# Kernel tuning notes

Measured on AMD Instinct MI355X. Metric: run time of the kernel, lower is better.

## Reference

```python
import jax, jax.numpy as jnp
import numpy as np


def setup_inputs() -> dict:
    key = jax.random.key(0)
    ks = jax.random.split(key, 7)
    S, A, I, H = 2000, 1000, 5, 32
    return {
        "g": jax.random.normal(ks[0], (S, A, I), dtype=jnp.float32),
        "W1": jax.random.normal(ks[1], (A, I, H), dtype=jnp.float32) * (1.0 / np.sqrt(I)),
        "b1": jax.random.normal(ks[2], (A, H), dtype=jnp.float32) * 0.01,
        "W2": jax.random.normal(ks[3], (A, H, H), dtype=jnp.float32) * (1.0 / np.sqrt(H)),
        "b2": jax.random.normal(ks[4], (A, H), dtype=jnp.float32) * 0.01,
        "W3": jax.random.normal(ks[5], (A, H, 1), dtype=jnp.float32) * (1.0 / np.sqrt(H)),
        "b3": jax.random.normal(ks[6], (A, 1), dtype=jnp.float32) * 0.01,
    }


def reference(g, W1, b1, W2, b2, W3, b3):
    # Batched equivalent of the nested per-struct / per-atom Python loop:
    # each atom `a` has its own tiny MLP (5 -> 32 -> 32 -> 1, tanh),
    # applied to g[s, a] for every structure s. Grouped-GEMM form:
    # s = struct, a = atom, i/h/o = feature dims.
    h1 = jnp.tanh(jnp.einsum('sai,aih->sah', g, W1) + b1[None, :, :])
    h2 = jnp.tanh(jnp.einsum('sah,aho->sao', h1, W2) + b2[None, :, :])
    e = jnp.einsum('sah,aho->sao', h2, W3) + b3[None, :, :]
    # e_nn has shape [n_struct, n_atoms], matching the torch buffer.
    return e[..., 0]
```

## Files before the change

### kernel.cpp

```cpp
#include <hip/hip_runtime.h>
#include <hip/hip_bf16.h>

#define NS_TOT 2000
#define NA 1000
#define NI 5
#define NH 32
#define SHALF 1000

typedef __attribute__((ext_vector_type(2)))  float f32x2;
typedef __attribute__((ext_vector_type(8)))  short short8;
typedef __attribute__((ext_vector_type(16))) float f32x16;

struct f4pair  { f32x2 a, b; };
struct accpair { f32x2 p[8]; };

__device__ __forceinline__ f32x2 tanh_pk(f32x2 X) {
    f32x2 z = X * X;
    f32x2 n = (z + 105.0f) * z + 945.0f;
    f32x2 d = (z * 15.0f + 420.0f) * z + 945.0f;
    f32x2 r;
    r.x = __builtin_amdgcn_rcpf(d.x);
    r.y = __builtin_amdgcn_rcpf(d.y);
    f32x2 t = X * n * r;
    t.x = __builtin_amdgcn_fmed3f(t.x, -1.0f, 1.0f);
    t.y = __builtin_amdgcn_fmed3f(t.y, -1.0f, 1.0f);
    return t;
}

__device__ __forceinline__ unsigned short f2bf_rne(float x) {
    unsigned u = __float_as_uint(x);
    unsigned r = u + 0x7FFFu + ((u >> 16) & 1u);
    return (unsigned short)(r >> 16);
}
__device__ __forceinline__ unsigned pack2(float a, float b) {
    __hip_bfloat162 p = __float22bfloat162_rn(make_float2(a, b));
    unsigned u; __builtin_memcpy(&u, &p, 4); return u;
}
__device__ __forceinline__ unsigned tanh2_pack(float a, float b) {
    f32x2 X = {a, b};
    f32x2 t = tanh_pk(X);
    return pack2(t.x, t.y);
}

__global__ __attribute__((amdgpu_flat_work_group_size(256, 256),
                          amdgpu_waves_per_eu(4, 8)))
void mlp_mfma(
    const float* __restrict__ g,
    const float* __restrict__ W1, const float* __restrict__ b1,
    const float* __restrict__ W2, const float* __restrict__ b2,
    const float* __restrict__ W3, const float* __restrict__ b3,
    float* __restrict__ out)
{
    const int bid   = blockIdx.x;
    const int araw  = bid % NA;
    const int chunk = bid / NA;
    const int a = (araw >> 3) + 125 * (araw & 7);
    const int t = threadIdx.x;
    const int lane = t & 63, wid = t >> 6;
    const int l31 = lane & 31, half = lane >> 5;

    const int sbase_blk = chunk * SHALF;
    const int send      = sbase_blk + SHALF;

    __shared__ __align__(16) unsigned short sW2T[NH * NH];
    __shared__ __align__(16) unsigned short sW1T[NH * 8];
    __shared__ __align__(16) float sB2[NH];
    __shared__ __align__(16) float sW3[NH];

    for (int idx = t; idx < NH * NH; idx += 256) {
        const int i = idx >> 5, j = idx & 31;
        sW2T[j * NH + i] = f2bf_rne(W2[(size_t)a * NH * NH + idx]);
    }
    if (t < NH) {
        sB2[t] = b2[a * NH + t];
        sW3[t] = W3[a * NH + t];
        const int m = t;
        #pragma unroll
        for (int i = 0; i < NI; ++i)
            sW1T[m * 8 + i] = f2bf_rne(W1[(size_t)a * NI * NH + i * NH + m]);
        sW1T[m * 8 + 5] = f2bf_rne(b1[a * NH + m]);
        sW1T[m * 8 + 6] = 0;
        sW1T[m * 8 + 7] = 0;
    }
    __syncthreads();

    const short8 zero8 = {0,0,0,0,0,0,0,0};
    const short8 w1ld = __builtin_bit_cast(short8, *(const uint4*)(sW1T + l31 * 8));
    const short8 afl1 = half ? zero8 : w1ld;
    const short8 af0 = __builtin_bit_cast(short8, *(const uint4*)(sW2T + l31 * NH + half * 8));
    const short8 af1 = __builtin_bit_cast(short8, *(const uint4*)(sW2T + l31 * NH + 16 + half * 8));
    const float4 b2q0 = ((const float4*)sB2)[0 + half];
    const float4 b2q1 = ((const float4*)sB2)[2 + half];
    const float4 b2q2 = ((const float4*)sB2)[4 + half];
    const float4 b2q3 = ((const float4*)sB2)[6 + half];
    const float4 w3q0 = ((const float4*)sW3)[0 + half];
    const float4 w3q1 = ((const float4*)sW3)[2 + half];
    const float4 w3q2 = ((const float4*)sW3)[4 + half];
    const float4 w3q3 = ((const float4*)sW3)[6 + half];
    const float bias3 = b3[a];
    const f4pair w3p0 = __builtin_bit_cast(f4pair, w3q0);
    const f4pair w3p1 = __builtin_bit_cast(f4pair, w3q1);
    const f4pair w3p2 = __builtin_bit_cast(f4pair, w3q2);
    const f4pair w3p3 = __builtin_bit_cast(f4pair, w3q3);
    const f32x16 zacc = {0,0,0,0,0,0,0,0,0,0,0,0,0,0,0,0};
    const f32x16 b2acc = {b2q0.x, b2q0.y, b2q0.z, b2q0.w,
                          b2q1.x, b2q1.y, b2q1.z, b2q1.w,
                          b2q2.x, b2q2.y, b2q2.z, b2q2.w,
                          b2q3.x, b2q3.y, b2q3.z, b2q3.w};

    float x0g, x1g, x2g, x3g, x4g;
    {
        const int s0 = sbase_blk + wid * 64 + lane;
        const int sl = (s0 < send) ? s0 : (send - 1);
        const float* gp = g + ((size_t)sl * NA + a) * NI;
        x0g = gp[0]; x1g = gp[1]; x2g = gp[2]; x3g = gp[3]; x4g = gp[4];
    }

    #pragma unroll
    for (int it = 0; it < 4; ++it) {
        const int base = sbase_blk + it * 256 + wid * 64;
        const int s = base + lane;

        float nx0, nx1, nx2, nx3, nx4;
        if (it < 3) {
            const int sn = s + 256;
            const int sln = (sn < send) ? sn : (send - 1);
            const float* gq = g + ((size_t)sln * NA + a) * NI;
            nx0 = gq[0]; nx1 = gq[1]; nx2 = gq[2]; nx3 = gq[3]; nx4 = gq[4];
        }

        const unsigned gp01 = pack2(x0g, x1g);
        const unsigned gp23 = pack2(x2g, x3g);
        const unsigned gp45 = pack2(x4g, 1.0f);
        auto gs01 = __builtin_amdgcn_permlane32_swap(gp01, gp01, false, false);
        auto gs23 = __builtin_amdgcn_permlane32_swap(gp23, gp23, false, false);
        auto gs45 = __builtin_amdgcn_permlane32_swap(gp45, gp45, false, false);
        const uint4 bu0 = make_uint4(gp01,    gp23,    gp45,    0u);
        const uint4 bu1 = make_uint4(gs01[1], gs23[1], gs45[1], 0u);
        const short8 gb0 = __builtin_bit_cast(short8, bu0);
        const short8 gb1 = __builtin_bit_cast(short8, bu1);

        f32x16 d0 = __builtin_amdgcn_mfma_f32_32x32x16_bf16(afl1, gb0, zacc, 0, 0, 0);
        f32x16 d1 = __builtin_amdgcn_mfma_f32_32x32x16_bf16(afl1, gb1, zacc, 0, 0, 0);

        short8 bk0_0, bk1_0, bk0_1, bk1_1;
        #define TILE_CONV(DD, BK0, BK1) { \
            const unsigned p0 = tanh2_pack(DD[0],  DD[1]); \
            const unsigned p1 = tanh2_pack(DD[2],  DD[3]); \
            const unsigned p2 = tanh2_pack(DD[4],  DD[5]); \
            const unsigned p3 = tanh2_pack(DD[6],  DD[7]); \
            const unsigned p4 = tanh2_pack(DD[8],  DD[9]); \
            const unsigned p5 = tanh2_pack(DD[10], DD[11]); \
            const unsigned p6 = tanh2_pack(DD[12], DD[13]); \
            const unsigned p7 = tanh2_pack(DD[14], DD[15]); \
            auto s02 = __builtin_amdgcn_permlane32_swap(p0, p2, false, false); \
            auto s13 = __builtin_amdgcn_permlane32_swap(p1, p3, false, false); \
            auto s46 = __builtin_amdgcn_permlane32_swap(p4, p6, false, false); \
            auto s57 = __builtin_amdgcn_permlane32_swap(p5, p7, false, false); \
            const uint4 u0 = make_uint4(s02[0], s13[0], s02[1], s13[1]); \
            const uint4 u1 = make_uint4(s46[0], s57[0], s46[1], s57[1]); \
            BK0 = __builtin_bit_cast(short8, u0); \
            BK1 = __builtin_bit_cast(short8, u1); }
        TILE_CONV(d0, bk0_0, bk1_0)
        TILE_CONV(d1, bk0_1, bk1_1)
        #undef TILE_CONV

        f32x16 acc0 = __builtin_amdgcn_mfma_f32_32x32x16_bf16(af0, bk0_0, b2acc, 0, 0, 0);
        acc0 = __builtin_amdgcn_mfma_f32_32x32x16_bf16(af1, bk1_0, acc0, 0, 0, 0);
        f32x16 acc1 = __builtin_amdgcn_mfma_f32_32x32x16_bf16(af0, bk0_1, b2acc, 0, 0, 0);
        acc1 = __builtin_amdgcn_mfma_f32_32x32x16_bf16(af1, bk1_1, acc1, 0, 0, 0);

        const accpair ap0 = __builtin_bit_cast(accpair, acc0);
        const accpair ap1 = __builtin_bit_cast(accpair, acc1);
        f32x2 p0 = {0.f, 0.f}, p1 = {0.f, 0.f};
        #define EPP(r, wpair) { \
            p0 += tanh_pk(ap0.p[r]) * (wpair); \
            p1 += tanh_pk(ap1.p[r]) * (wpair); }
        EPP(0, w3p0.a) EPP(1, w3p0.b)
        EPP(2, w3p1.a) EPP(3, w3p1.b)
        EPP(4, w3p2.a) EPP(5, w3p2.b)
        EPP(6, w3p3.a) EPP(7, w3p3.b)
        #undef EPP
        const float e0 = p0.x + p0.y;
        const float e1 = p1.x + p1.y;
        auto es = __builtin_amdgcn_permlane32_swap(__float_as_uint(e0),
                                                   __float_as_uint(e1),
                                                   false, false);
        const float etot = __uint_as_float(es[0]) + __uint_as_float(es[1]);
        if (s < send) out[(size_t)s * NA + a] = etot + bias3;

        if (it < 3) { x0g = nx0; x1g = nx1; x2g = nx2; x3g = nx3; x4g = nx4; }
    }
}

extern "C" void kernel_launch(void* const* d_in, const int* in_sizes, int n_in,
                              void* d_out, int out_size, void* d_ws, size_t ws_size,
                              hipStream_t stream) {
    const float* g  = (const float*)d_in[0];
    const float* W1 = (const float*)d_in[1];
    const float* b1 = (const float*)d_in[2];
    const float* W2 = (const float*)d_in[3];
    const float* b2 = (const float*)d_in[4];
    const float* W3 = (const float*)d_in[5];
    const float* b3 = (const float*)d_in[6];
    float* out = (float*)d_out;
    mlp_mfma<<<dim3(NA * 2), dim3(256), 0, stream>>>(g, W1, b1, W2, b2, W3, b3, out);
}
```

Measured before the change: 120.9 us.

## Software-pipeline layer-1 MFMA and deepen g prefetch; pad W2 LDS rows

Restructures the per-iteration loop so the layer-1 MFMA for the next tile is issued while the current tile's tanh epilogue runs. The g loads are now prefetched two iterations ahead instead of one. The W2 LDS tile gets a padded row stride of 40 to avoid bank conflicts on the transpose writes and fragment reads. The occupancy hint is lowered to 3-4 waves per EU to give the deeper pipeline more registers, at the cost of fewer resident waves.

```diff
diff --git a/kernel.cpp b/kernel.cpp
--- a/kernel.cpp
+++ b/kernel.cpp
@@ -6,6 +6,7 @@
 #define NI 5
 #define NH 32
 #define SHALF 1000
+#define W2LD 40
 
 typedef __attribute__((ext_vector_type(2)))  float f32x2;
 typedef __attribute__((ext_vector_type(8)))  short short8;
@@ -43,7 +44,7 @@
 }
 
 __global__ __attribute__((amdgpu_flat_work_group_size(256, 256),
-                          amdgpu_waves_per_eu(4, 8)))
+                          amdgpu_waves_per_eu(3, 4)))
 void mlp_mfma(
     const float* __restrict__ g,
     const float* __restrict__ W1, const float* __restrict__ b1,
@@ -62,14 +63,14 @@
     const int sbase_blk = chunk * SHALF;
     const int send      = sbase_blk + SHALF;
 
-    __shared__ __align__(16) unsigned short sW2T[NH * NH];
+    __shared__ __align__(16) unsigned short sW2T[NH * W2LD];
     __shared__ __align__(16) unsigned short sW1T[NH * 8];
     __shared__ __align__(16) float sB2[NH];
     __shared__ __align__(16) float sW3[NH];
 
     for (int idx = t; idx < NH * NH; idx += 256) {
         const int i = idx >> 5, j = idx & 31;
-        sW2T[j * NH + i] = f2bf_rne(W2[(size_t)a * NH * NH + idx]);
+        sW2T[j * W2LD + i] = f2bf_rne(W2[(size_t)a * NH * NH + idx]);
     }
     if (t < NH) {
         sB2[t] = b2[a * NH + t];
@@ -87,8 +88,8 @@
     const short8 zero8 = {0,0,0,0,0,0,0,0};
     const short8 w1ld = __builtin_bit_cast(short8, *(const uint4*)(sW1T + l31 * 8));
     const short8 afl1 = half ? zero8 : w1ld;
-    const short8 af0 = __builtin_bit_cast(short8, *(const uint4*)(sW2T + l31 * NH + half * 8));
-    const short8 af1 = __builtin_bit_cast(short8, *(const uint4*)(sW2T + l31 * NH + 16 + half * 8));
+    const short8 af0 = __builtin_bit_cast(short8, *(const uint4*)(sW2T + l31 * W2LD + half * 8));
+    const short8 af1 = __builtin_bit_cast(short8, *(const uint4*)(sW2T + l31 * W2LD + 16 + half * 8));
     const float4 b2q0 = ((const float4*)sB2)[0 + half];
     const float4 b2q1 = ((const float4*)sB2)[2 + half];
     const float4 b2q2 = ((const float4*)sB2)[4 + half];
@@ -108,40 +109,37 @@
                           b2q2.x, b2q2.y, b2q2.z, b2q2.w,
                           b2q3.x, b2q3.y, b2q3.z, b2q3.w};
 
+    #define BUILD_L1(AX0, AX1, AX2, AX3, AX4) { \
+        const unsigned gp01 = pack2(AX0, AX1); \
+        const unsigned gp23 = pack2(AX2, AX3); \
+        const unsigned gp45 = pack2(AX4, 1.0f); \
+        auto gs01 = __builtin_amdgcn_permlane32_swap(gp01, gp01, false, false); \
+        auto gs23 = __builtin_amdgcn_permlane32_swap(gp23, gp23, false, false); \
+        auto gs45 = __builtin_amdgcn_permlane32_swap(gp45, gp45, false, false); \
+        const uint4 bu0 = make_uint4(gp01,    gp23,    gp45,    0u); \
+        const uint4 bu1 = make_uint4(gs01[1], gs23[1], gs45[1], 0u); \
+        const short8 gb0 = __builtin_bit_cast(short8, bu0); \
+        const short8 gb1 = __builtin_bit_cast(short8, bu1); \
+        d0 = __builtin_amdgcn_mfma_f32_32x32x16_bf16(afl1, gb0, zacc, 0, 0, 0); \
+        d1 = __builtin_amdgcn_mfma_f32_32x32x16_bf16(afl1, gb1, zacc, 0, 0, 0); }
+
     float x0g, x1g, x2g, x3g, x4g;
+    float y0g, y1g, y2g, y3g, y4g;
     {
         const int s0 = sbase_blk + wid * 64 + lane;
-        const int sl = (s0 < send) ? s0 : (send - 1);
-        const float* gp = g + ((size_t)sl * NA + a) * NI;
+        const float* gp = g + ((size_t)s0 * NA + a) * NI;
         x0g = gp[0]; x1g = gp[1]; x2g = gp[2]; x3g = gp[3]; x4g = gp[4];
-    }
+        const int s1 = s0 + 256;
+        const float* gq = g + ((size_t)s1 * NA + a) * NI;
+        y0g = gq[0]; y1g = gq[1]; y2g = gq[2]; y3g = gq[3]; y4g = gq[4];
+    }
+    f32x16 d0, d1;
+    BUILD_L1(x0g, x1g, x2g, x3g, x4g)
 
     #pragma unroll
     for (int it = 0; it < 4; ++it) {
         const int base = sbase_blk + it * 256 + wid * 64;
         const int s = base + lane;
-
-        float nx0, nx1, nx2, nx3, nx4;
-        if (it < 3) {
-            const int sn = s + 256;
-            const int sln = (sn < send) ? sn : (send - 1);
-            const float* gq = g + ((size_t)sln * NA + a) * NI;
-            nx0 = gq[0]; nx1 = gq[1]; nx2 = gq[2]; nx3 = gq[3]; nx4 = gq[4];
-        }
-
-        const unsigned gp01 = pack2(x0g, x1g);
-        const unsigned gp23 = pack2(x2g, x3g);
-        const unsigned gp45 = pack2(x4g, 1.0f);
-        auto gs01 = __builtin_amdgcn_permlane32_swap(gp01, gp01, false, false);
-        auto gs23 = __builtin_amdgcn_permlane32_swap(gp23, gp23, false, false);
-        auto gs45 = __builtin_amdgcn_permlane32_swap(gp45, gp45, false, false);
-        const uint4 bu0 = make_uint4(gp01,    gp23,    gp45,    0u);
-        const uint4 bu1 = make_uint4(gs01[1], gs23[1], gs45[1], 0u);
-        const short8 gb0 = __builtin_bit_cast(short8, bu0);
-        const short8 gb1 = __builtin_bit_cast(short8, bu1);
-
-        f32x16 d0 = __builtin_amdgcn_mfma_f32_32x32x16_bf16(afl1, gb0, zacc, 0, 0, 0);
-        f32x16 d1 = __builtin_amdgcn_mfma_f32_32x32x16_bf16(afl1, gb1, zacc, 0, 0, 0);
 
         short8 bk0_0, bk1_0, bk0_1, bk1_1;
         #define TILE_CONV(DD, BK0, BK1) { \
@@ -170,27 +168,37 @@
         f32x16 acc1 = __builtin_amdgcn_mfma_f32_32x32x16_bf16(af0, bk0_1, b2acc, 0, 0, 0);
         acc1 = __builtin_amdgcn_mfma_f32_32x32x16_bf16(af1, bk1_1, acc1, 0, 0, 0);
 
+        if (it < 3) {
+            BUILD_L1(y0g, y1g, y2g, y3g, y4g)
+        }
+        if (it < 2) {
+            const int sn = s + 512;
+            const int sln = (sn < send) ? sn : (send - 1);
+            const float* gq = g + ((size_t)sln * NA + a) * NI;
+            y0g = gq[0]; y1g = gq[1]; y2g = gq[2]; y3g = gq[3]; y4g = gq[4];
+        }
+
         const accpair ap0 = __builtin_bit_cast(accpair, acc0);
+        f32x2 p0 = {0.f, 0.f};
+        p0 += tanh_pk(ap0.p[0]) * w3p0.a;  p0 += tanh_pk(ap0.p[1]) * w3p0.b;
+        p0 += tanh_pk(ap0.p[2]) * w3p1.a;  p0 += tanh_pk(ap0.p[3]) * w3p1.b;
+        p0 += tanh_pk(ap0.p[4]) * w3p2.a;  p0 += tanh_pk(ap0.p[5]) * w3p2.b;
+        p0 += tanh_pk(ap0.p[6]) * w3p3.a;  p0 += tanh_pk(ap0.p[7]) * w3p3.b;
+        const float e0 = p0.x + p0.y;
         const accpair ap1 = __builtin_bit_cast(accpair, acc1);
-        f32x2 p0 = {0.f, 0.f}, p1 = {0.f, 0.f};
-        #define EPP(r, wpair) { \
-            p0 += tanh_pk(ap0.p[r]) * (wpair); \
-            p1 += tanh_pk(ap1.p[r]) * (wpair); }
-        EPP(0, w3p0.a) EPP(1, w3p0.b)
-        EPP(2, w3p1.a) EPP(3, w3p1.b)
-        EPP(4, w3p2.a) EPP(5, w3p2.b)
-        EPP(6, w3p3.a) EPP(7, w3p3.b)
-        #undef EPP
-        const float e0 = p0.x + p0.y;
+        f32x2 p1 = {0.f, 0.f};
+        p1 += tanh_pk(ap1.p[0]) * w3p0.a;  p1 += tanh_pk(ap1.p[1]) * w3p0.b;
+        p1 += tanh_pk(ap1.p[2]) * w3p1.a;  p1 += tanh_pk(ap1.p[3]) * w3p1.b;
+        p1 += tanh_pk(ap1.p[4]) * w3p2.a;  p1 += tanh_pk(ap1.p[5]) * w3p2.b;
+        p1 += tanh_pk(ap1.p[6]) * w3p3.a;  p1 += tanh_pk(ap1.p[7]) * w3p3.b;
         const float e1 = p1.x + p1.y;
         auto es = __builtin_amdgcn_permlane32_swap(__float_as_uint(e0),
                                                    __float_as_uint(e1),
                                                    false, false);
         const float etot = __uint_as_float(es[0]) + __uint_as_float(es[1]);
         if (s < send) out[(size_t)s * NA + a] = etot + bias3;
-
-        if (it < 3) { x0g = nx0; x1g = nx1; x2g = nx2; x3g = nx3; x4g = nx4; }
-    }
+    }
+    #undef BUILD_L1
 }
 
 extern "C" void kernel_launch(void* const* d_in, const int* in_sizes, int n_in,
```

Result: no change. 120.5 us (-0.3%).

## Process eight atoms per block with vectorized g loads and output stores

Applied to the files above, without the earlier changes.

Reassigns each block to a group of eight consecutive atoms over a 125-structure chunk, so each lane loads its structure's 40 contiguous g floats with float4 loads and writes eight outputs with two float4 stores. This replaces the strided per-atom scalar gathers and scattered 4-byte stores. Weights for all eight atoms are staged in padded LDS, and the shared tanh reciprocal is computed once per pair. It raises register use and per-block weight staging, and the merged reciprocal can lose accuracy or overflow for large inputs.

```diff
diff --git a/kernel.cpp b/kernel.cpp
--- a/kernel.cpp
+++ b/kernel.cpp
@@ -5,7 +5,10 @@
 #define NA 1000
 #define NI 5
 #define NH 32
-#define SHALF 1000
+#define NATB 8
+#define NCHUNK 16
+#define SCHUNK 125
+#define W2LD 40
 
 typedef __attribute__((ext_vector_type(2)))  float f32x2;
 typedef __attribute__((ext_vector_type(8)))  short short8;
@@ -18,9 +21,10 @@
     f32x2 z = X * X;
     f32x2 n = (z + 105.0f) * z + 945.0f;
     f32x2 d = (z * 15.0f + 420.0f) * z + 945.0f;
+    const float rr = __builtin_amdgcn_rcpf(d.x * d.y);
     f32x2 r;
-    r.x = __builtin_amdgcn_rcpf(d.x);
-    r.y = __builtin_amdgcn_rcpf(d.y);
+    r.x = rr * d.y;
+    r.y = rr * d.x;
     f32x2 t = X * n * r;
     t.x = __builtin_amdgcn_fmed3f(t.x, -1.0f, 1.0f);
     t.y = __builtin_amdgcn_fmed3f(t.y, -1.0f, 1.0f);
@@ -43,7 +47,7 @@
 }
 
 __global__ __attribute__((amdgpu_flat_work_group_size(256, 256),
-                          amdgpu_waves_per_eu(4, 8)))
+                          amdgpu_waves_per_eu(3, 4)))
 void mlp_mfma(
     const float* __restrict__ g,
     const float* __restrict__ W1, const float* __restrict__ b1,
@@ -51,145 +55,134 @@
     const float* __restrict__ W3, const float* __restrict__ b3,
     float* __restrict__ out)
 {
-    const int bid   = blockIdx.x;
-    const int araw  = bid % NA;
-    const int chunk = bid / NA;
-    const int a = (araw >> 3) + 125 * (araw & 7);
+    const int bid  = blockIdx.x;
+    const int swz  = (bid & 7) * 250 + (bid >> 3);
+    const int grp  = swz >> 4;
+    const int chunk= swz & 15;
+    const int a0   = grp * NATB;
+
     const int t = threadIdx.x;
     const int lane = t & 63, wid = t >> 6;
     const int l31 = lane & 31, half = lane >> 5;
 
-    const int sbase_blk = chunk * SHALF;
-    const int send      = sbase_blk + SHALF;
-
-    __shared__ __align__(16) unsigned short sW2T[NH * NH];
-    __shared__ __align__(16) unsigned short sW1T[NH * 8];
-    __shared__ __align__(16) float sB2[NH];
-    __shared__ __align__(16) float sW3[NH];
-
-    for (int idx = t; idx < NH * NH; idx += 256) {
-        const int i = idx >> 5, j = idx & 31;
-        sW2T[j * NH + i] = f2bf_rne(W2[(size_t)a * NH * NH + idx]);
-    }
-    if (t < NH) {
-        sB2[t] = b2[a * NH + t];
-        sW3[t] = W3[a * NH + t];
-        const int m = t;
+    __shared__ __align__(16) unsigned short sW1T[NATB * 64 * 8];
+    __shared__ __align__(16) unsigned short sW2T[NATB * NH * W2LD];
+    __shared__ __align__(16) float sB2f[NATB * NH];
+    __shared__ __align__(16) float sW3f[NATB * NH];
+
+    for (int idx = t; idx < NATB * NH * NH; idx += 256) {
+        const int jat = idx >> 10, e = idx & 1023, k = e >> 5, m = e & 31;
+        sW2T[jat * (NH * W2LD) + m * W2LD + k] =
+            f2bf_rne(W2[(size_t)(a0 + jat) * NH * NH + e]);
+    }
+    {
+        const int jat = t >> 5, m = t & 31;
+        const int rbase = jat * 512 + m * 8;
         #pragma unroll
         for (int i = 0; i < NI; ++i)
-            sW1T[m * 8 + i] = f2bf_rne(W1[(size_t)a * NI * NH + i * NH + m]);
-        sW1T[m * 8 + 5] = f2bf_rne(b1[a * NH + m]);
-        sW1T[m * 8 + 6] = 0;
-        sW1T[m * 8 + 7] = 0;
+            sW1T[rbase + i] = f2bf_rne(W1[(size_t)(a0 + jat) * NI * NH + i * NH + m]);
+        sW1T[rbase + 5] = f2bf_rne(b1[(a0 + jat) * NH + m]);
+        sW1T[rbase + 6] = 0;
+        sW1T[rbase + 7] = 0;
+        *(uint4*)(sW1T + jat * 512 + 256 + m * 8) = make_uint4(0, 0, 0, 0);
+        sB2f[t] = b2[(a0 + jat) * NH + m];
+        sW3f[t] = W3[(a0 + jat) * NH + m];
     }
     __syncthreads();
 
-    const short8 zero8 = {0,0,0,0,0,0,0,0};
-    const short8 w1ld = __builtin_bit_cast(short8, *(const uint4*)(sW1T + l31 * 8));
-    const short8 afl1 = half ? zero8 : w1ld;
-    const short8 af0 = __builtin_bit_cast(short8, *(const uint4*)(sW2T + l31 * NH + half * 8));
-    const short8 af1 = __builtin_bit_cast(short8, *(const uint4*)(sW2T + l31 * NH + 16 + half * 8));
-    const float4 b2q0 = ((const float4*)sB2)[0 + half];
-    const float4 b2q1 = ((const float4*)sB2)[2 + half];
-    const float4 b2q2 = ((const float4*)sB2)[4 + half];
-    const float4 b2q3 = ((const float4*)sB2)[6 + half];
-    const float4 w3q0 = ((const float4*)sW3)[0 + half];
-    const float4 w3q1 = ((const float4*)sW3)[2 + half];
-    const float4 w3q2 = ((const float4*)sW3)[4 + half];
-    const float4 w3q3 = ((const float4*)sW3)[6 + half];
-    const float bias3 = b3[a];
-    const f4pair w3p0 = __builtin_bit_cast(f4pair, w3q0);
-    const f4pair w3p1 = __builtin_bit_cast(f4pair, w3q1);
-    const f4pair w3p2 = __builtin_bit_cast(f4pair, w3q2);
-    const f4pair w3p3 = __builtin_bit_cast(f4pair, w3q3);
+    const int sblk  = chunk * SCHUNK;
+    const int slast = sblk + SCHUNK - 1;
+    const int s     = sblk + wid * 32 + l31;
+    const int sl    = (s < slast) ? s : slast;
+
+    const float* gp = g + ((size_t)sl * NA + a0) * NI;
+    float gf[40];
+    #pragma unroll
+    for (int q = 0; q < 10; ++q) {
+        const float4 v = ((const float4*)gp)[q];
+        gf[4*q+0] = v.x; gf[4*q+1] = v.y; gf[4*q+2] = v.z; gf[4*q+3] = v.w;
+    }
+    unsigned gw[24];
+    #pragma unroll
+    for (int j = 0; j < NATB; ++j) {
+        gw[3*j+0] = pack2(gf[5*j+0], gf[5*j+1]);
+        gw[3*j+1] = pack2(gf[5*j+2], gf[5*j+3]);
+        gw[3*j+2] = pack2(gf[5*j+4], 1.0f);
+    }
+
+    const float4 b3q0 = *(const float4*)(b3 + a0);
+    const float4 b3q1 = *(const float4*)(b3 + a0 + 4);
+    const float b3v[8] = {b3q0.x, b3q0.y, b3q0.z, b3q0.w,
+                          b3q1.x, b3q1.y, b3q1.z, b3q1.w};
+
     const f32x16 zacc = {0,0,0,0,0,0,0,0,0,0,0,0,0,0,0,0};
-    const f32x16 b2acc = {b2q0.x, b2q0.y, b2q0.z, b2q0.w,
-                          b2q1.x, b2q1.y, b2q1.z, b2q1.w,
-                          b2q2.x, b2q2.y, b2q2.z, b2q2.w,
-                          b2q3.x, b2q3.y, b2q3.z, b2q3.w};
-
-    float x0g, x1g, x2g, x3g, x4g;
-    {
-        const int s0 = sbase_blk + wid * 64 + lane;
-        const int sl = (s0 < send) ? s0 : (send - 1);
-        const float* gp = g + ((size_t)sl * NA + a) * NI;
-        x0g = gp[0]; x1g = gp[1]; x2g = gp[2]; x3g = gp[3]; x4g = gp[4];
-    }
+    float eres[8];
 
     #pragma unroll
-    for (int it = 0; it < 4; ++it) {
-        const int base = sbase_blk + it * 256 + wid * 64;
-        const int s = base + lane;
-
-        float nx0, nx1, nx2, nx3, nx4;
-        if (it < 3) {
-            const int sn = s + 256;
-            const int sln = (sn < send) ? sn : (send - 1);
-            const float* gq = g + ((size_t)sln * NA + a) * NI;
-            nx0 = gq[0]; nx1 = gq[1]; nx2 = gq[2]; nx3 = gq[3]; nx4 = gq[4];
+    for (int jat = 0; jat < NATB; ++jat) {
+        const short8 afl1 = __builtin_bit_cast(short8,
+            *(const uint4*)(sW1T + jat * 512 + lane * 8));
+        const uint4 bu0 = make_uint4(gw[3*jat], gw[3*jat+1], gw[3*jat+2], 0u);
+        const short8 gb0 = __builtin_bit_cast(short8, bu0);
+        const f32x16 d = __builtin_amdgcn_mfma_f32_32x32x16_bf16(afl1, gb0, zacc, 0, 0, 0);
+
+        short8 bk0, bk1;
+        {
+            const unsigned p0 = tanh2_pack(d[0],  d[1]);
+            const unsigned p1 = tanh2_pack(d[2],  d[3]);
+            const unsigned p2 = tanh2_pack(d[4],  d[5]);
+            const unsigned p3 = tanh2_pack(d[6],  d[7]);
+            const unsigned p4 = tanh2_pack(d[8],  d[9]);
+            const unsigned p5 = tanh2_pack(d[10], d[11]);
+            const unsigned p6 = tanh2_pack(d[12], d[13]);
+            const unsigned p7 = tanh2_pack(d[14], d[15]);
+            auto s02 = __builtin_amdgcn_permlane32_swap(p0, p2, false, false);
+            auto s13 = __builtin_amdgcn_permlane32_swap(p1, p3, false, false);
+            auto s46 = __builtin_amdgcn_permlane32_swap(p4, p6, false, false);
+            auto s57 = __builtin_amdgcn_permlane32_swap(p5, p7, false, false);
+            const uint4 u0 = make_uint4(s02[0], s13[0], s02[1], s13[1]);
+            const uint4 u1 = make_uint4(s46[0], s57[0], s46[1], s57[1]);
+            bk0 = __builtin_bit_cast(short8, u0);
+            bk1 = __builtin_bit_cast(short8, u1);
         }
 
-        const unsigned gp01 = pack2(x0g, x1g);
-        const unsigned gp23 = pack2(x2g, x3g);
-        const unsigned gp45 = pack2(x4g, 1.0f);
-        auto gs01 = __builtin_amdgcn_permlane32_swap(gp01, gp01, false, false);
-        auto gs23 = __builtin_amdgcn_permlane32_swap(gp23, gp23, false, false);
-        auto gs45 = __builtin_amdgcn_permlane32_swap(gp45, gp45, false, false);
-        const uint4 bu0 = make_uint4(gp01,    gp23,    gp45,    0u);
-        const uint4 bu1 = make_uint4(gs01[1], gs23[1], gs45[1], 0u);
-        const short8 gb0 = __builtin_bit_cast(short8, bu0);
-        const short8 gb1 = __builtin_bit_cast(short8, bu1);
-
-        f32x16 d0 = __builtin_amdgcn_mfma_f32_32x32x16_bf16(afl1, gb0, zacc, 0, 0, 0);
-        f32x16 d1 = __builtin_amdgcn_mfma_f32_32x32x16_bf16(afl1, gb1, zacc, 0, 0, 0);
-
-        short8 bk0_0, bk1_0, bk0_1, bk1_1;
-        #define TILE_CONV(DD, BK0, BK1) { \
-            const unsigned p0 = tanh2_pack(DD[0],  DD[1]); \
-            const unsigned p1 = tanh2_pack(DD[2],  DD[3]); \
-            const unsigned p2 = tanh2_pack(DD[4],  DD[5]); \
-            const unsigned p3 = tanh2_pack(DD[6],  DD[7]); \
-            const unsigned p4 = tanh2_pack(DD[8],  DD[9]); \
-            const unsigned p5 = tanh2_pack(DD[10], DD[11]); \
-            const unsigned p6 = tanh2_pack(DD[12], DD[13]); \
-            const unsigned p7 = tanh2_pack(DD[14], DD[15]); \
-            auto s02 = __builtin_amdgcn_permlane32_swap(p0, p2, false, false); \
-            auto s13 = __builtin_amdgcn_permlane32_swap(p1, p3, false, false); \
-            auto s46 = __builtin_amdgcn_permlane32_swap(p4, p6, false, false); \
-            auto s57 = __builtin_amdgcn_permlane32_swap(p5, p7, false, false); \
-            const uint4 u0 = make_uint4(s02[0], s13[0], s02[1], s13[1]); \
-            const uint4 u1 = make_uint4(s46[0], s57[0], s46[1], s57[1]); \
-            BK0 = __builtin_bit_cast(short8, u0); \
-            BK1 = __builtin_bit_cast(short8, u1); }
-        TILE_CONV(d0, bk0_0, bk1_0)
-        TILE_CONV(d1, bk0_1, bk1_1)
-        #undef TILE_CONV
-
-        f32x16 acc0 = __builtin_amdgcn_mfma_f32_32x32x16_bf16(af0, bk0_0, b2acc, 0, 0, 0);
-        acc0 = __builtin_amdgcn_mfma_f32_32x32x16_bf16(af1, bk1_0, acc0, 0, 0, 0);
-        f32x16 acc1 = __builtin_amdgcn_mfma_f32_32x32x16_bf16(af0, bk0_1, b2acc, 0, 0, 0);
-        acc1 = __builtin_amdgcn_mfma_f32_32x32x16_bf16(af1, bk1_1, acc1, 0, 0, 0);
-
-        const accpair ap0 = __builtin_bit_cast(accpair, acc0);
-        const accpair ap1 = __builtin_bit_cast(accpair, acc1);
-        f32x2 p0 = {0.f, 0.f}, p1 = {0.f, 0.f};
-        #define EPP(r, wpair) { \
-            p0 += tanh_pk(ap0.p[r]) * (wpair); \
-            p1 += tanh_pk(ap1.p[r]) * (wpair); }
-        EPP(0, w3p0.a) EPP(1, w3p0.b)
-        EPP(2, w3p1.a) EPP(3, w3p1.b)
-        EPP(4, w3p2.a) EPP(5, w3p2.b)
-        EPP(6, w3p3.a) EPP(7, w3p3.b)
-        #undef EPP
-        const float e0 = p0.x + p0.y;
-        const float e1 = p1.x + p1.y;
-        auto es = __builtin_amdgcn_permlane32_swap(__float_as_uint(e0),
-                                                   __float_as_uint(e1),
+        const float* b2p = sB2f + jat * NH;
+        const float4 q0 = ((const float4*)b2p)[0 + half];
+        const float4 q1 = ((const float4*)b2p)[2 + half];
+        const float4 q2 = ((const float4*)b2p)[4 + half];
+        const float4 q3 = ((const float4*)b2p)[6 + half];
+        const f32x16 b2a = {q0.x, q0.y, q0.z, q0.w, q1.x, q1.y, q1.z, q1.w,
+                            q2.x, q2.y, q2.z, q2.w, q3.x, q3.y, q3.z, q3.w};
+        const unsigned short* w2p = sW2T + jat * (NH * W2LD) + l31 * W2LD + half * 8;
+        const short8 af0 = __builtin_bit_cast(short8, *(const uint4*)w2p);
+        const short8 af1 = __builtin_bit_cast(short8, *(const uint4*)(w2p + 16));
+        f32x16 acc = __builtin_amdgcn_mfma_f32_32x32x16_bf16(af0, bk0, b2a, 0, 0, 0);
+        acc = __builtin_amdgcn_mfma_f32_32x32x16_bf16(af1, bk1, acc, 0, 0, 0);
+
+        const float* w3b = sW3f + jat * NH;
+        const f4pair w3p0 = __builtin_bit_cast(f4pair, ((const float4*)w3b)[0 + half]);
+        const f4pair w3p1 = __builtin_bit_cast(f4pair, ((const float4*)w3b)[2 + half]);
+        const f4pair w3p2 = __builtin_bit_cast(f4pair, ((const float4*)w3b)[4 + half]);
+        const f4pair w3p3 = __builtin_bit_cast(f4pair, ((const float4*)w3b)[6 + half]);
+        const accpair ap = __builtin_bit_cast(accpair, acc);
+        f32x2 p = {0.f, 0.f};
+        p += tanh_pk(ap.p[0]) * w3p0.a;  p += tanh_pk(ap.p[1]) * w3p0.b;
+        p += tanh_pk(ap.p[2]) * w3p1.a;  p += tanh_pk(ap.p[3]) * w3p1.b;
+        p += tanh_pk(ap.p[4]) * w3p2.a;  p += tanh_pk(ap.p[5]) * w3p2.b;
+        p += tanh_pk(ap.p[6]) * w3p3.a;  p += tanh_pk(ap.p[7]) * w3p3.b;
+        const float e = p.x + p.y;
+        auto es = __builtin_amdgcn_permlane32_swap(__float_as_uint(e),
+                                                   __float_as_uint(e),
                                                    false, false);
-        const float etot = __uint_as_float(es[0]) + __uint_as_float(es[1]);
-        if (s < send) out[(size_t)s * NA + a] = etot + bias3;
-
-        if (it < 3) { x0g = nx0; x1g = nx1; x2g = nx2; x3g = nx3; x4g = nx4; }
+        eres[jat] = __uint_as_float(es[0]) + __uint_as_float(es[1]) + b3v[jat];
+    }
+
+    if (half == 0 && s <= slast) {
+        const float4 o0 = {eres[0], eres[1], eres[2], eres[3]};
+        const float4 o1 = {eres[4], eres[5], eres[6], eres[7]};
+        float* op = out + (size_t)s * NA + a0;
+        *(float4*)op       = o0;
+        *(float4*)(op + 4) = o1;
     }
 }
 
@@ -204,5 +197,5 @@
     const float* W3 = (const float*)d_in[5];
     const float* b3 = (const float*)d_in[6];
     float* out = (float*)d_out;
-    mlp_mfma<<<dim3(NA * 2), dim3(256), 0, stream>>>(g, W1, b1, W2, b2, W3, b3, out);
-}
+    mlp_mfma<<<dim3(125 * NCHUNK), dim3(256), 0, stream>>>(g, W1, b1, W2, b2, W3, b3, out);
+}
```

Result: slower. 125.7 us (+4.0%).
